# Kernel optimization log

Measured on AMD Instinct MI355X. Metric: run time of the kernel, lower is better.

## Reference

```python
import jax, jax.numpy as jnp
import numpy as np

B, S, D, H = 2, 2048, 1024, 16
HD = D // H  # head dim = 64


def setup_inputs() -> dict:
    key = jax.random.key(0)
    ks = jax.random.split(key, 5)
    scale = 1.0 / np.sqrt(D)
    return {
        "hidden_states": jax.random.normal(ks[0], (B, S, D), jnp.float32),
        "attention_mask": jax.random.normal(ks[1], (B, 1, 1, S), jnp.float32),
        "Wq": jax.random.normal(ks[2], (D, D), jnp.float32) * scale,
        "bq": jnp.zeros((D,), jnp.float32),
        "Wk": jax.random.normal(ks[3], (D, D), jnp.float32) * scale,
        "bk": jnp.zeros((D,), jnp.float32),
        "Wv": jax.random.normal(ks[4], (D, D), jnp.float32) * scale,
        "bv": jnp.zeros((D,), jnp.float32),
    }


def _split_heads(x):
    # [B,S,D] -> [B,H,S,HD]
    return x.reshape(B, S, H, HD).transpose(0, 2, 1, 3)


def reference(hidden_states, attention_mask, Wq, bq, Wk, bk, Wv, bv):
    # torch Linear: y = x @ W.T + b
    q = _split_heads(hidden_states @ Wq.T + bq)
    k = _split_heads(hidden_states @ Wk.T + bk)
    v = _split_heads(hidden_states @ Wv.T + bv)

    scores = jnp.einsum("bhqd,bhkd->bhqk", q, k)
    # Faithful to source: with a mask present, the 1/sqrt(head_dim) scaling
    # is overwritten and raw scores are multiplied by the binary key mask.
    mask = (attention_mask >= 0).astype(scores.dtype)  # [B,1,1,S]
    probs = scores * mask
    # dropout prob = 0 (eval) -> identity

    ctx = jnp.einsum("bhqk,bhkd->bhqd", probs, v)
    ctx = ctx.transpose(0, 2, 1, 3).reshape(B, S, D)
    return ctx
```

## Files before the change

kernel.cpp:

```cpp
#include <hip/hip_runtime.h>

#define BB 2
#define SS 2048
#define DD 1024
#define HH 16
#define HDIM 64
#define MTOT 4096

typedef unsigned short u16;
typedef __bf16 bf16_t;
typedef bf16_t bf16x8 __attribute__((ext_vector_type(8)));
typedef float floatx4 __attribute__((ext_vector_type(4)));
typedef float floatx16 __attribute__((ext_vector_type(16)));

__device__ __forceinline__ float bf2f(u16 u) {
  union { unsigned int i; float f; } x;
  x.i = ((unsigned int)u) << 16;
  return x.f;
}
__device__ __forceinline__ u16 f2bf(float f) {
  union { float f; unsigned int i; } x;
  x.f = f;
  unsigned int r = x.i + 0x7fffu + ((x.i >> 16) & 1u);
  return (u16)(r >> 16);
}

__device__ __forceinline__ void gload16(const u16* g, u16* l) {
  __builtin_amdgcn_global_load_lds(
      (const __attribute__((address_space(1))) unsigned int*)g,
      (__attribute__((address_space(3))) unsigned int*)l, 16, 0, 0);
}

__global__ __launch_bounds__(256) void cast_to_bf16(
    const float* __restrict__ hs, const float* __restrict__ wq,
    const float* __restrict__ wk, const float* __restrict__ wv,
    u16* __restrict__ hs_b, u16* __restrict__ wq_b,
    u16* __restrict__ wk_b, u16* __restrict__ wv_b) {
  int fid = blockIdx.x * 256 + threadIdx.x;
  const float* src;
  u16* dst;
  int local;
  if (fid < 1048576) { src = hs; dst = hs_b; local = fid; }
  else if (fid < 1310720) { src = wq; dst = wq_b; local = fid - 1048576; }
  else if (fid < 1572864) { src = wk; dst = wk_b; local = fid - 1310720; }
  else { src = wv; dst = wv_b; local = fid - 1572864; }
  float4 v = reinterpret_cast<const float4*>(src)[local];
  ushort4 o;
  o.x = f2bf(v.x); o.y = f2bf(v.y); o.z = f2bf(v.z); o.w = f2bf(v.w);
  reinterpret_cast<ushort4*>(dst)[local] = o;
}

#define BKK 32
__global__ __launch_bounds__(256) void qkv_gemm_kernel(
    const u16* __restrict__ A,
    const u16* __restrict__ Wq, const u16* __restrict__ Wk, const u16* __restrict__ Wv,
    const float* __restrict__ bq, const float* __restrict__ bk, const float* __restrict__ bv,
    u16* __restrict__ Qo, u16* __restrict__ Ko, u16* __restrict__ Vo) {
  __shared__ u16 sA[3][128 * BKK];
  __shared__ u16 sB[3][128 * BKK];
  const int mt = blockIdx.y, ntall = blockIdx.x;
  const int seg = ntall >> 3, nt = ntall & 7;
  const u16* Wp = (seg == 0) ? Wq : (seg == 1) ? Wk : Wv;
  const float* bp = (seg == 0) ? bq : (seg == 1) ? bk : bv;
  u16* Out = (seg == 0) ? Qo : (seg == 1) ? Ko : Vo;
  const int m0 = mt * 128, n0 = nt * 128;
  const int tid = threadIdx.x;
  const int lane = tid & 63, wave = tid >> 6;
  const int wm = (wave >> 1) * 64, wn = (wave & 1) * 64;
  const int l32 = lane & 31, khalf = lane >> 5;
  const int srow0 = wave * 32 + (lane >> 2);
  const int scol = (lane & 3) * 8;

#define STAGE(buf, kbase)                                                    \
  {                                                                          \
    _Pragma("unroll") for (int c = 0; c < 2; ++c) {                          \
      int r = srow0 + c * 16;                                                \
      gload16(A + (size_t)(m0 + r) * DD + (kbase) + scol,                    \
              sA[buf] + r * BKK + scol);                                     \
      gload16(Wp + (size_t)(n0 + r) * DD + (kbase) + scol,                   \
              sB[buf] + r * BKK + scol);                                     \
    }                                                                        \
  }

  floatx16 acc[2][2] = {};
  STAGE(0, 0);
  STAGE(1, BKK);
  asm volatile("s_waitcnt vmcnt(4)" ::: "memory");
  asm volatile("s_barrier" ::: "memory");

  int cur = 0;
  for (int t = 0; t < 32; ++t) {
    if (t < 30) {
      int nb = cur + 2;
      if (nb >= 3) nb -= 3;
      STAGE(nb, (t + 2) * BKK);
    }
    const u16* pA = sA[cur];
    const u16* pB = sB[cur];
#pragma unroll
    for (int kk = 0; kk < 2; ++kk) {
      bf16x8 af[2], bfr[2];
#pragma unroll
      for (int i = 0; i < 2; ++i)
        af[i] = *reinterpret_cast<const bf16x8*>(pA + (wm + i * 32 + l32) * BKK + kk * 16 + khalf * 8);
#pragma unroll
      for (int j = 0; j < 2; ++j)
        bfr[j] = *reinterpret_cast<const bf16x8*>(pB + (wn + j * 32 + l32) * BKK + kk * 16 + khalf * 8);
#pragma unroll
      for (int i = 0; i < 2; ++i)
#pragma unroll
        for (int j = 0; j < 2; ++j)
          acc[i][j] = __builtin_amdgcn_mfma_f32_32x32x16_bf16(af[i], bfr[j], acc[i][j], 0, 0, 0);
    }
    if (t < 30) asm volatile("s_waitcnt vmcnt(4)" ::: "memory");
    else if (t == 30) asm volatile("s_waitcnt vmcnt(0)" ::: "memory");
    if (t < 31) asm volatile("s_barrier" ::: "memory");
    cur = (cur < 2) ? cur + 1 : 0;
  }
#undef STAGE

#pragma unroll
  for (int j = 0; j < 2; ++j) {
    int col = n0 + wn + j * 32 + l32;
    float bias = bp[col];
#pragma unroll
    for (int i = 0; i < 2; ++i) {
#pragma unroll
      for (int reg = 0; reg < 16; ++reg) {
        int row = m0 + wm + i * 32 + (reg & 3) + 8 * (reg >> 2) + 4 * khalf;
        Out[(size_t)row * DD + col] = f2bf(acc[i][j][reg] + bias);
      }
    }
  }
}

__global__ __launch_bounds__(256) void m_partial_kernel(
    const u16* __restrict__ Xb, const u16* __restrict__ Yb,
    const float* __restrict__ am, float* __restrict__ mpart) {
  __shared__ float sX[64 * 68];
  __shared__ float sY[64 * 68];
  const int bh = blockIdx.y;
  const int b = bh >> 4, h = bh & 15;
  const int tid = threadIdx.x;
  const int e0 = (tid & 15) * 4, d0 = (tid >> 4) * 4;
  float acc[4][4] = {};
  for (int cs = 0; cs < 4; ++cs) {
    const int s0 = (blockIdx.x * 4 + cs) * 64;
    if (cs) __syncthreads();
#pragma unroll
    for (int c = 0; c < 2; ++c) {
      int L = tid + c * 256;
      int srow = L >> 3;
      int col = (L & 7) * 8;
      size_t g = (size_t)(b * SS + s0 + srow) * DD + h * HDIM + col;
      uint4 xraw = *reinterpret_cast<const uint4*>(Xb + g);
      uint4 yraw = *reinterpret_cast<const uint4*>(Yb + g);
      float m = (am[b * SS + s0 + srow] >= 0.f) ? 1.f : 0.f;
      unsigned int xw[4] = {xraw.x, xraw.y, xraw.z, xraw.w};
      unsigned int yw[4] = {yraw.x, yraw.y, yraw.z, yraw.w};
#pragma unroll
      for (int q = 0; q < 4; ++q) {
        sX[srow * 68 + col + 2 * q]     = m * bf2f((u16)(xw[q] & 0xffffu));
        sX[srow * 68 + col + 2 * q + 1] = m * bf2f((u16)(xw[q] >> 16));
        sY[srow * 68 + col + 2 * q]     = bf2f((u16)(yw[q] & 0xffffu));
        sY[srow * 68 + col + 2 * q + 1] = bf2f((u16)(yw[q] >> 16));
      }
    }
    __syncthreads();
    for (int s = 0; s < 64; ++s) {
      float4 xx = *reinterpret_cast<const float4*>(&sX[s * 68 + e0]);
      float4 yy = *reinterpret_cast<const float4*>(&sY[s * 68 + d0]);
      float xa[4] = {xx.x, xx.y, xx.z, xx.w};
      float ya[4] = {yy.x, yy.y, yy.z, yy.w};
#pragma unroll
      for (int i = 0; i < 4; ++i)
#pragma unroll
        for (int j = 0; j < 4; ++j) acc[i][j] += xa[i] * ya[j];
    }
  }
  float* outp = mpart + ((size_t)(blockIdx.x * 32 + bh)) * 4096;
#pragma unroll
  for (int i = 0; i < 4; ++i) {
    float4 o = {acc[i][0], acc[i][1], acc[i][2], acc[i][3]};
    *reinterpret_cast<float4*>(&outp[(e0 + i) * 64 + d0]) = o;
  }
}

__global__ __launch_bounds__(256) void ctx_kernel(
    const u16* __restrict__ Qb, const float* __restrict__ mpart, float* __restrict__ Out) {
  __shared__ u16 sMT[64 * 72];
  const int m0 = blockIdx.x * 128;
  const int h = blockIdx.y;
  const int b = m0 >> 11;
  const int bh = b * HH + h;
  const int tid = threadIdx.x;
#pragma unroll
  for (int c = 0; c < 4; ++c) {
    int L4 = c * 256 + tid;
    float4 s = {0.f, 0.f, 0.f, 0.f};
#pragma unroll
    for (int pc = 0; pc < 8; ++pc) {
      const float4* p4 = reinterpret_cast<const float4*>(mpart + ((size_t)(pc * 32 + bh)) * 4096);
      float4 t = p4[L4];
      s.x += t.x; s.y += t.y; s.z += t.z; s.w += t.w;
    }
    int d = L4 >> 4, e = (L4 & 15) * 4;
    ushort4 o = {f2bf(s.x), f2bf(s.y), f2bf(s.z), f2bf(s.w)};
    *reinterpret_cast<ushort4*>(&sMT[d * 72 + e]) = o;
  }
  __syncthreads();
  const int lane = tid & 63, wave = tid >> 6;
  const int l32 = lane & 31, khalf = lane >> 5;
  const int arow = m0 + wave * 32 + l32;
  const u16* qrow = Qb + (size_t)arow * DD + h * HDIM + khalf * 8;
  bf16x8 af[4], bfr[2][4];
#pragma unroll
  for (int k0 = 0; k0 < 4; ++k0) {
    af[k0] = *reinterpret_cast<const bf16x8*>(qrow + k0 * 16);
#pragma unroll
    for (int j = 0; j < 2; ++j)
      bfr[j][k0] = *reinterpret_cast<const bf16x8*>(
          &sMT[(j * 32 + l32) * 72 + k0 * 16 + khalf * 8]);
  }
  floatx16 acc[2] = {};
#pragma unroll
  for (int j = 0; j < 2; ++j)
#pragma unroll
    for (int k0 = 0; k0 < 4; ++k0)
      acc[j] = __builtin_amdgcn_mfma_f32_32x32x16_bf16(af[k0], bfr[j][k0], acc[j], 0, 0, 0);
#pragma unroll
  for (int j = 0; j < 2; ++j) {
    int col = h * HDIM + j * 32 + l32;
#pragma unroll
    for (int reg = 0; reg < 16; ++reg) {
      int r = m0 + wave * 32 + (reg & 3) + 8 * (reg >> 2) + 4 * khalf;
      Out[(size_t)r * DD + col] = acc[j][reg];
    }
  }
}

extern "C" void kernel_launch(void* const* d_in, const int* in_sizes, int n_in,
                              void* d_out, int out_size, void* d_ws, size_t ws_size,
                              hipStream_t stream) {
  const float* hs = (const float*)d_in[0];
  const float* am = (const float*)d_in[1];
  const float* wq = (const float*)d_in[2];
  const float* bq = (const float*)d_in[3];
  const float* wk = (const float*)d_in[4];
  const float* bk = (const float*)d_in[5];
  const float* wv = (const float*)d_in[6];
  const float* bv = (const float*)d_in[7];
  float* out = (float*)d_out;
  char* ws = (char*)d_ws;

  u16* hs_b = (u16*)(ws);
  u16* wq_b = (u16*)(ws + 8388608);
  u16* wk_b = (u16*)(ws + 10485760);
  u16* wv_b = (u16*)(ws + 12582912);
  u16* q_b  = (u16*)(ws + 14680064);
  u16* k_b  = (u16*)(ws + 23068672);
  u16* v_b  = (u16*)(ws + 31457280);
  float* mpart = (float*)(ws + 39845888);

  cast_to_bf16<<<7168, 256, 0, stream>>>(hs, wq, wk, wv, hs_b, wq_b, wk_b, wv_b);
  qkv_gemm_kernel<<<dim3(24, 32), 256, 0, stream>>>(hs_b, wq_b, wk_b, wv_b,
                                                    bq, bk, bv, q_b, k_b, v_b);
  m_partial_kernel<<<dim3(8, 32), 256, 0, stream>>>(v_b, k_b, am, mpart);
  ctx_kernel<<<dim3(32, 16), 256, 0, stream>>>(q_b, mpart, out);
}
```

Measured before the change: 151.5 us.

## Fuse fp32-to-bf16 cast into QKV GEMM with register-prefetched loads

Removes the separate cast kernel and has the QKV GEMM read fp32 inputs and weights directly, converting to bf16 in registers before storing to LDS. The three-stage async global-to-LDS pipeline is replaced by a single LDS buffer with a one-step register prefetch, plus two barriers per k-step. This saves one launch and the extra write and read of the bf16 copies. The GEMM now reads twice the bytes per tile, redoes the conversion in every block that shares a tile, and the single-buffered LDS gives less overlap between loads and MFMA work.

```diff
diff --git a/kernel.cpp b/kernel.cpp
--- a/kernel.cpp
+++ b/kernel.cpp
@@ -10,6 +10,7 @@
 typedef unsigned short u16;
 typedef __bf16 bf16_t;
 typedef bf16_t bf16x8 __attribute__((ext_vector_type(8)));
+typedef u16 u16x8 __attribute__((ext_vector_type(8)));
 typedef float floatx4 __attribute__((ext_vector_type(4)));
 typedef float floatx16 __attribute__((ext_vector_type(16)));
 
@@ -25,42 +26,24 @@
   return (u16)(r >> 16);
 }
 
-__device__ __forceinline__ void gload16(const u16* g, u16* l) {
-  __builtin_amdgcn_global_load_lds(
-      (const __attribute__((address_space(1))) unsigned int*)g,
-      (__attribute__((address_space(3))) unsigned int*)l, 16, 0, 0);
-}
-
-__global__ __launch_bounds__(256) void cast_to_bf16(
-    const float* __restrict__ hs, const float* __restrict__ wq,
-    const float* __restrict__ wk, const float* __restrict__ wv,
-    u16* __restrict__ hs_b, u16* __restrict__ wq_b,
-    u16* __restrict__ wk_b, u16* __restrict__ wv_b) {
-  int fid = blockIdx.x * 256 + threadIdx.x;
-  const float* src;
-  u16* dst;
-  int local;
-  if (fid < 1048576) { src = hs; dst = hs_b; local = fid; }
-  else if (fid < 1310720) { src = wq; dst = wq_b; local = fid - 1048576; }
-  else if (fid < 1572864) { src = wk; dst = wk_b; local = fid - 1310720; }
-  else { src = wv; dst = wv_b; local = fid - 1572864; }
-  float4 v = reinterpret_cast<const float4*>(src)[local];
-  ushort4 o;
-  o.x = f2bf(v.x); o.y = f2bf(v.y); o.z = f2bf(v.z); o.w = f2bf(v.w);
-  reinterpret_cast<ushort4*>(dst)[local] = o;
+__device__ __forceinline__ u16x8 pack8(float4 a, float4 b) {
+  u16x8 o;
+  o[0] = f2bf(a.x); o[1] = f2bf(a.y); o[2] = f2bf(a.z); o[3] = f2bf(a.w);
+  o[4] = f2bf(b.x); o[5] = f2bf(b.y); o[6] = f2bf(b.z); o[7] = f2bf(b.w);
+  return o;
 }
 
 #define BKK 32
-__global__ __launch_bounds__(256) void qkv_gemm_kernel(
-    const u16* __restrict__ A,
-    const u16* __restrict__ Wq, const u16* __restrict__ Wk, const u16* __restrict__ Wv,
+__global__ __launch_bounds__(256, 2) void qkv_fused_kernel(
+    const float* __restrict__ A32,
+    const float* __restrict__ Wq, const float* __restrict__ Wk, const float* __restrict__ Wv,
     const float* __restrict__ bq, const float* __restrict__ bk, const float* __restrict__ bv,
     u16* __restrict__ Qo, u16* __restrict__ Ko, u16* __restrict__ Vo) {
-  __shared__ u16 sA[3][128 * BKK];
-  __shared__ u16 sB[3][128 * BKK];
+  __shared__ u16 sA[128 * BKK];
+  __shared__ u16 sB[128 * BKK];
   const int mt = blockIdx.y, ntall = blockIdx.x;
   const int seg = ntall >> 3, nt = ntall & 7;
-  const u16* Wp = (seg == 0) ? Wq : (seg == 1) ? Wk : Wv;
+  const float* Wp = (seg == 0) ? Wq : (seg == 1) ? Wk : Wv;
   const float* bp = (seg == 0) ? bq : (seg == 1) ? bk : bv;
   u16* Out = (seg == 0) ? Qo : (seg == 1) ? Ko : Vo;
   const int m0 = mt * 128, n0 = nt * 128;
@@ -70,54 +53,62 @@
   const int l32 = lane & 31, khalf = lane >> 5;
   const int srow0 = wave * 32 + (lane >> 2);
   const int scol = (lane & 3) * 8;
-
-#define STAGE(buf, kbase)                                                    \
-  {                                                                          \
-    _Pragma("unroll") for (int c = 0; c < 2; ++c) {                          \
-      int r = srow0 + c * 16;                                                \
-      gload16(A + (size_t)(m0 + r) * DD + (kbase) + scol,                    \
-              sA[buf] + r * BKK + scol);                                     \
-      gload16(Wp + (size_t)(n0 + r) * DD + (kbase) + scol,                   \
-              sB[buf] + r * BKK + scol);                                     \
-    }                                                                        \
-  }
+  const float* pa0 = A32 + (size_t)(m0 + srow0) * DD + scol;
+  const float* pa1 = A32 + (size_t)(m0 + srow0 + 16) * DD + scol;
+  const float* pw0 = Wp + (size_t)(n0 + srow0) * DD + scol;
+  const float* pw1 = Wp + (size_t)(n0 + srow0 + 16) * DD + scol;
+
+  float4 pre[8];
+  pre[0] = *reinterpret_cast<const float4*>(pa0);
+  pre[1] = *reinterpret_cast<const float4*>(pa0 + 4);
+  pre[2] = *reinterpret_cast<const float4*>(pa1);
+  pre[3] = *reinterpret_cast<const float4*>(pa1 + 4);
+  pre[4] = *reinterpret_cast<const float4*>(pw0);
+  pre[5] = *reinterpret_cast<const float4*>(pw0 + 4);
+  pre[6] = *reinterpret_cast<const float4*>(pw1);
+  pre[7] = *reinterpret_cast<const float4*>(pw1 + 4);
 
   floatx16 acc[2][2] = {};
-  STAGE(0, 0);
-  STAGE(1, BKK);
-  asm volatile("s_waitcnt vmcnt(4)" ::: "memory");
-  asm volatile("s_barrier" ::: "memory");
-
-  int cur = 0;
   for (int t = 0; t < 32; ++t) {
-    if (t < 30) {
-      int nb = cur + 2;
-      if (nb >= 3) nb -= 3;
-      STAGE(nb, (t + 2) * BKK);
-    }
-    const u16* pA = sA[cur];
-    const u16* pB = sB[cur];
+    u16x8 wa0 = pack8(pre[0], pre[1]);
+    u16x8 wa1 = pack8(pre[2], pre[3]);
+    u16x8 wb0 = pack8(pre[4], pre[5]);
+    u16x8 wb1 = pack8(pre[6], pre[7]);
+    asm volatile("s_barrier" ::: "memory");
+    *reinterpret_cast<u16x8*>(sA + srow0 * BKK + scol) = wa0;
+    *reinterpret_cast<u16x8*>(sA + (srow0 + 16) * BKK + scol) = wa1;
+    *reinterpret_cast<u16x8*>(sB + srow0 * BKK + scol) = wb0;
+    *reinterpret_cast<u16x8*>(sB + (srow0 + 16) * BKK + scol) = wb1;
+    if (t < 31) {
+      const int k1 = (t + 1) * BKK;
+      pre[0] = *reinterpret_cast<const float4*>(pa0 + k1);
+      pre[1] = *reinterpret_cast<const float4*>(pa0 + k1 + 4);
+      pre[2] = *reinterpret_cast<const float4*>(pa1 + k1);
+      pre[3] = *reinterpret_cast<const float4*>(pa1 + k1 + 4);
+      pre[4] = *reinterpret_cast<const float4*>(pw0 + k1);
+      pre[5] = *reinterpret_cast<const float4*>(pw0 + k1 + 4);
+      pre[6] = *reinterpret_cast<const float4*>(pw1 + k1);
+      pre[7] = *reinterpret_cast<const float4*>(pw1 + k1 + 4);
+    }
+    asm volatile("s_waitcnt lgkmcnt(0)" ::: "memory");
+    asm volatile("s_barrier" ::: "memory");
+    __builtin_amdgcn_sched_barrier(0);
 #pragma unroll
     for (int kk = 0; kk < 2; ++kk) {
       bf16x8 af[2], bfr[2];
 #pragma unroll
       for (int i = 0; i < 2; ++i)
-        af[i] = *reinterpret_cast<const bf16x8*>(pA + (wm + i * 32 + l32) * BKK + kk * 16 + khalf * 8);
+        af[i] = *reinterpret_cast<const bf16x8*>(sA + (wm + i * 32 + l32) * BKK + kk * 16 + khalf * 8);
 #pragma unroll
       for (int j = 0; j < 2; ++j)
-        bfr[j] = *reinterpret_cast<const bf16x8*>(pB + (wn + j * 32 + l32) * BKK + kk * 16 + khalf * 8);
+        bfr[j] = *reinterpret_cast<const bf16x8*>(sB + (wn + j * 32 + l32) * BKK + kk * 16 + khalf * 8);
 #pragma unroll
       for (int i = 0; i < 2; ++i)
 #pragma unroll
         for (int j = 0; j < 2; ++j)
           acc[i][j] = __builtin_amdgcn_mfma_f32_32x32x16_bf16(af[i], bfr[j], acc[i][j], 0, 0, 0);
     }
-    if (t < 30) asm volatile("s_waitcnt vmcnt(4)" ::: "memory");
-    else if (t == 30) asm volatile("s_waitcnt vmcnt(0)" ::: "memory");
-    if (t < 31) asm volatile("s_barrier" ::: "memory");
-    cur = (cur < 2) ? cur + 1 : 0;
-  }
-#undef STAGE
+  }
 
 #pragma unroll
   for (int j = 0; j < 2; ++j) {
@@ -253,18 +244,13 @@
   float* out = (float*)d_out;
   char* ws = (char*)d_ws;
 
-  u16* hs_b = (u16*)(ws);
-  u16* wq_b = (u16*)(ws + 8388608);
-  u16* wk_b = (u16*)(ws + 10485760);
-  u16* wv_b = (u16*)(ws + 12582912);
-  u16* q_b  = (u16*)(ws + 14680064);
-  u16* k_b  = (u16*)(ws + 23068672);
-  u16* v_b  = (u16*)(ws + 31457280);
-  float* mpart = (float*)(ws + 39845888);
-
-  cast_to_bf16<<<7168, 256, 0, stream>>>(hs, wq, wk, wv, hs_b, wq_b, wk_b, wv_b);
-  qkv_gemm_kernel<<<dim3(24, 32), 256, 0, stream>>>(hs_b, wq_b, wk_b, wv_b,
-                                                    bq, bk, bv, q_b, k_b, v_b);
+  u16* q_b  = (u16*)(ws);
+  u16* k_b  = (u16*)(ws + 8388608);
+  u16* v_b  = (u16*)(ws + 16777216);
+  float* mpart = (float*)(ws + 25165824);
+
+  qkv_fused_kernel<<<dim3(24, 32), 256, 0, stream>>>(hs, wq, wk, wv,
+                                                     bq, bk, bv, q_b, k_b, v_b);
   m_partial_kernel<<<dim3(8, 32), 256, 0, stream>>>(v_b, k_b, am, mpart);
   ctx_kernel<<<dim3(32, 16), 256, 0, stream>>>(q_b, mpart, out);
 }
```

Result: no change. 151.6 us (+0.0%).
